# Optimization experiments

Measured on AMD Instinct MI355X. Metric: run time of the kernel, lower is better.

The kernel has to match this reference:

```python
import jax, jax.numpy as jnp
import numpy as np

GRID_SIZE = 5
ORDER = 3  # spline_order
H_STEP = 2.0 / GRID_SIZE  # grid_range = [-1, 1]
GRID = jnp.arange(-ORDER, GRID_SIZE + ORDER + 1, dtype=jnp.float32) * H_STEP - 1.0  # (12,)


def b_splines(x):
    # x: (N, F) -> bases: (N, F, GRID_SIZE + ORDER) via Cox-de Boor recursion
    g = GRID
    xx = x[..., None]
    bases = ((xx >= g[:-1]) & (xx < g[1:])).astype(x.dtype)
    for k in range(1, ORDER + 1):
        left = (xx - g[:-(k + 1)]) / (g[k:-1] - g[:-(k + 1)]) * bases[..., :-1]
        right = (g[k + 1:] - xx) / (g[k + 1:] - g[1:-k]) * bases[..., 1:]
        bases = left + right
    return bases


def kan_linear(x, bw, sw, sc):
    # x: (N, F); bw: (O, F); sw: (O, F, C); sc: (O, F)
    base = jax.nn.silu(x) @ bw.T
    spline = jnp.einsum('nfc,ofc->no', b_splines(x), sw * sc[..., None])
    return base + spline


def kan_conv(x, bw, sw, sc):
    # x: (B, C, H, W); 3x3 patches, padding 1, stride 1 -> KANLinear over C*9 features
    B, C, H, W = x.shape
    patches = jax.lax.conv_general_dilated_patches(x, (3, 3), (1, 1), ((1, 1), (1, 1)))  # (B, C*9, H, W)
    p = patches.transpose(0, 2, 3, 1).reshape(B * H * W, C * 9)
    o = kan_linear(p, bw, sw, sc)  # (B*H*W, Cout)
    return o.reshape(B, H, W, -1).transpose(0, 3, 1, 2)


def maxpool2(x):
    B, C, H, W = x.shape
    return x.reshape(B, C, H // 2, 2, W // 2, 2).max(axis=(3, 5))


def setup_inputs() -> dict:
    key = jax.random.key(0)
    ks = jax.random.split(key, 32)
    d = {}
    d['x'] = jax.random.normal(ks[0], (128, 3, 32, 32), dtype=jnp.float32)
    conv_specs = [(3, 4), (4, 8), (8, 16), (16, 32)]
    i = 1
    for li, (cin, cout) in enumerate(conv_specs, 1):
        fin = cin * 9
        d[f'bw{li}'] = jax.random.normal(ks[i], (cout, fin), dtype=jnp.float32) * (1.0 / np.sqrt(fin)); i += 1
        d[f'sw{li}'] = jax.random.normal(ks[i], (cout, fin, GRID_SIZE + ORDER), dtype=jnp.float32) * 0.1; i += 1
        d[f'sc{li}'] = jax.random.normal(ks[i], (cout, fin), dtype=jnp.float32) * (1.0 / np.sqrt(fin)); i += 1
    lin_specs = [(2048, 2048), (1024, 2048), (10, 1024)]
    for li, (o, inn) in enumerate(lin_specs, 1):
        d[f'w{li}'] = jax.random.normal(ks[i], (o, inn), dtype=jnp.float32) * (1.0 / np.sqrt(inn)); i += 1
        d[f'b{li}'] = jnp.zeros((o,), dtype=jnp.float32); i += 1
    return d


def reference(x, bw1, sw1, sc1, bw2, sw2, sc2, bw3, sw3, sc3, bw4, sw4, sc4, w1, b1, w2, b2, w3, b3):
    x = kan_conv(x, bw1, sw1, sc1)
    x = kan_conv(x, bw2, sw2, sc2)
    x = maxpool2(x)
    x = kan_conv(x, bw3, sw3, sc3)
    x = kan_conv(x, bw4, sw4, sc4)
    x = maxpool2(x)
    x = x.reshape(x.shape[0], -1)  # (B, 32*8*8)
    x = jax.nn.relu(x @ w1.T + b1)
    x = jax.nn.relu(x @ w2.T + b2)
    return x @ w3.T + b3
```

## Files before the change

kernel.cpp:

```cpp
#include <hip/hip_runtime.h>

#define BATCH 128
#define AST 88

typedef __attribute__((ext_vector_type(8))) short bf16x8;
typedef __attribute__((ext_vector_type(16))) float f32x16;

__device__ __forceinline__ void spline_acts(float xv, float act[9]) {
    act[0] = xv * (1.0f / (1.0f + __expf(-xv)));
    float g[12];
#pragma unroll
    for (int i = 0; i < 12; ++i) g[i] = (float)(i - 3) * 0.4f - 1.0f;
    float bb[11];
#pragma unroll
    for (int c = 0; c < 11; ++c) bb[c] = (xv >= g[c] && xv < g[c + 1]) ? 1.0f : 0.0f;
#pragma unroll
    for (int k = 1; k <= 3; ++k) {
#pragma unroll
        for (int c = 0; c + k < 11; ++c) {
            float left  = (xv - g[c]) * (1.0f / (g[c + k] - g[c])) * bb[c];
            float right = (g[c + k + 1] - xv) * (1.0f / (g[c + k + 1] - g[c + 1])) * bb[c + 1];
            bb[c] = left + right;
        }
    }
#pragma unroll
    for (int c = 0; c < 8; ++c) act[c + 1] = bb[c];
}

__device__ __constant__ float ZPAD[9] = {0.0f, 0.0f, 0.0f, 0.02083333333f,
                                         0.47916666667f, 0.47916666667f,
                                         0.02083333333f, 0.0f, 0.0f};

__device__ __forceinline__ void bf16split(float x, ushort& h, ushort& l) {
    union { float f; unsigned u; } a; a.f = x;
    unsigned r = a.u + 0x7FFF + ((a.u >> 16) & 1);
    h = (ushort)(r >> 16);
    union { unsigned u; float f; } hf; hf.u = (unsigned)h << 16;
    union { float f; unsigned u; } bres; bres.f = x - hf.f;
    unsigned r2 = bres.u + 0x7FFF + ((bres.u >> 16) & 1);
    l = (ushort)(r2 >> 16);
}

__device__ __forceinline__ float wval(const float* bw, const float* sw, const float* sc,
                                      int F, int f, int j, int o) {
    if (j == 0) return bw[o * F + f];
    return sw[(o * F + f) * 8 + (j - 1)] * sc[o * F + f];
}

__global__ void pack_frags(
    const float* __restrict__ bw1, const float* __restrict__ sw1, const float* __restrict__ sc1,
    const float* __restrict__ bw2, const float* __restrict__ sw2, const float* __restrict__ sc2,
    const float* __restrict__ bw3, const float* __restrict__ sw3, const float* __restrict__ sc3,
    const float* __restrict__ bw4, const float* __restrict__ sw4, const float* __restrict__ sc4,
    ushort* __restrict__ k1h, ushort* __restrict__ k1l,
    ushort* __restrict__ k2h, ushort* __restrict__ k2l,
    ushort* __restrict__ k3h, ushort* __restrict__ k3l,
    ushort* __restrict__ k4h, ushort* __restrict__ k4l,
    ushort* __restrict__ zph, ushort* __restrict__ zpl) {
    int i = blockIdx.x * 256 + threadIdx.x;
    if (i < 1152) {
        int l = i & 63, s = (i >> 6) & 1, t = i / 128;
#pragma unroll
        for (int e = 0; e < 8; ++e) {
            int k = s * 16 + ((l >> 5) * 8) + e, o = l & 31;
            float w = 0.f;
            if (k < 27 && o < 4) w = wval(bw1, sw1, sc1, 27, (k / 9) * 9 + t, k % 9, o);
            ushort h, lo; bf16split(w, h, lo);
            k1h[i * 8 + e] = h; k1l[i * 8 + e] = lo;
        }
    } else if (i < 2880) {
        int q = i - 1152;
        int l = q & 63, s = (q >> 6) % 3, t = q / 192;
#pragma unroll
        for (int e = 0; e < 8; ++e) {
            int k = s * 16 + ((l >> 5) * 8) + e, o = l & 31;
            float w = 0.f;
            if (k < 36 && o < 8) w = wval(bw2, sw2, sc2, 36, (k / 9) * 9 + t, k % 9, o);
            ushort h, lo; bf16split(w, h, lo);
            k2h[q * 8 + e] = h; k2l[q * 8 + e] = lo;
        }
    } else if (i < 5760) {
        int q = i - 2880;
        int l = q & 63, s = (q >> 6) % 5, t = q / 320;
#pragma unroll
        for (int e = 0; e < 8; ++e) {
            int k = s * 16 + ((l >> 5) * 8) + e, o = l & 31;
            float w = 0.f;
            if (k < 72 && o < 16) w = wval(bw3, sw3, sc3, 72, (k / 9) * 9 + t, k % 9, o);
            ushort h, lo; bf16split(w, h, lo);
            k3h[q * 8 + e] = h; k3l[q * 8 + e] = lo;
        }
    } else if (i < 11520) {
        int q = i - 5760;
        int l = q & 63, s = (q >> 6) % 5, t = (q / 320) % 9, p = q / 2880;
#pragma unroll
        for (int e = 0; e < 8; ++e) {
            int k = s * 16 + ((l >> 5) * 8) + e, o = l & 31;
            float w = 0.f;
            if (k < 72) w = wval(bw4, sw4, sc4, 144, (p * 8 + k / 9) * 9 + t, k % 9, o);
            ushort h, lo; bf16split(w, h, lo);
            k4h[q * 8 + e] = h; k4l[q * 8 + e] = lo;
        }
    } else if (i < 11600) {
        int c = i - 11520;
        ushort h, lo; bf16split(ZPAD[c % 9], h, lo);
        zph[c] = h; zpl[c] = lo;
    }
}

__global__ __launch_bounds__(256) void spline_x(const float* __restrict__ x,
                                                ushort* __restrict__ A1h,
                                                ushort* __restrict__ A1l) {
    __shared__ unsigned SB[7168];
    int i = blockIdx.x * 256 + threadIdx.x;
    int px = i & 1023, b = i >> 10;
    const float* xb = x + (size_t)b * 3072 + px;
    unsigned rh[14] = {}, rl[14] = {};
#pragma unroll
    for (int cin = 0; cin < 3; ++cin) {
        float a9[9];
        spline_acts(xb[cin * 1024], a9);
#pragma unroll
        for (int j = 0; j < 9; ++j) {
            ushort h, l2; bf16split(a9[j], h, l2);
            int c = cin * 9 + j;
            if (c & 1) { rh[c >> 1] |= (unsigned)h << 16; rl[c >> 1] |= (unsigned)l2 << 16; }
            else       { rh[c >> 1] |= h;                  rl[c >> 1] |= l2; }
        }
    }
    int wb = threadIdx.x * 14;
#pragma unroll
    for (int w = 0; w < 14; ++w) { SB[wb + w] = rh[w]; SB[3584 + wb + w] = rl[w]; }
    __syncthreads();
    const ushort* sb = (const ushort*)SB;
    size_t base = (size_t)blockIdx.x * 7168;
#pragma unroll
    for (int e = 0; e < 4; ++e) {
        int q = e * 256 + threadIdx.x;
        if (q < 896) {
            *(uint4*)(A1h + base + q * 8) = *(const uint4*)(sb + q * 8);
            *(uint4*)(A1l + base + q * 8) = *(const uint4*)(sb + 7168 + q * 8);
        }
    }
}

template <int KG, int CHG, int CHL, int ASTR, int KSTEPS, int NCO, int EPI>
__global__ __launch_bounds__(256) void conv_strip(
    const ushort* __restrict__ Agh, const ushort* __restrict__ Agl,
    const ushort* __restrict__ Bgh, const ushort* __restrict__ Bgl,
    const ushort* __restrict__ zph, const ushort* __restrict__ zpl,
    ushort* __restrict__ Oh, ushort* __restrict__ Ol) {
    __shared__ ushort AH[340 * ASTR];
    __shared__ ushort AL[340 * ASTR];
    const int tid = threadIdx.x;
    const int b = blockIdx.x >> 2, strip = blockIdx.x & 3;
    const int r0 = strip * 8;
    const int lane = tid & 63, wv = tid >> 6;

    {
        const ushort* ash = Agh + (size_t)b * 1024 * KG;
        const ushort* asl = Agl + (size_t)b * 1024 * KG;
        for (int idx = tid; idx < 320 * CHL; idx += 256) {
            int pxl = idx / CHL, ch = idx - pxl * CHL;
            int lr = pxl >> 5, c = pxl & 31;
            int grow = r0 - 1 + lr;
            uint2 vh, vl;
            if (ch >= CHG) { vh = make_uint2(0u, 0u); vl = make_uint2(0u, 0u); }
            else if ((unsigned)grow < 32u) {
                vh = *(const uint2*)(ash + (size_t)(grow * 32 + c) * KG + ch * 4);
                vl = *(const uint2*)(asl + (size_t)(grow * 32 + c) * KG + ch * 4);
            } else {
                vh = *(const uint2*)(zph + ch * 4);
                vl = *(const uint2*)(zpl + ch * 4);
            }
            int spx = lr * 34 + c + 1;
            *(uint2*)(&AH[spx * ASTR + ch * 4]) = vh;
            *(uint2*)(&AL[spx * ASTR + ch * 4]) = vl;
        }
        for (int idx = tid; idx < 20 * CHL; idx += 256) {
            int sel = idx / CHL, ch = idx - sel * CHL;
            int lr = sel >> 1, c = (sel & 1) ? 33 : 0;
            int spx = lr * 34 + c;
            uint2 vh, vl;
            if (ch >= CHG) { vh = make_uint2(0u, 0u); vl = make_uint2(0u, 0u); }
            else { vh = *(const uint2*)(zph + ch * 4); vl = *(const uint2*)(zpl + ch * 4); }
            *(uint2*)(&AH[spx * ASTR + ch * 4]) = vh;
            *(uint2*)(&AL[spx * ASTR + ch * 4]) = vl;
        }
    }
    __syncthreads();

    f32x16 acc0, acc1;
#pragma unroll
    for (int i = 0; i < 16; ++i) { acc0[i] = 0.f; acc1[i] = 0.f; }

    const int p0 = wv * 64 + (lane & 31);
    const int sp0 = ((p0 >> 5) + 1) * 34 + (p0 & 31) + 1;
    const int sp1 = sp0 + 34;
    const int koff = (lane >> 5) * 8;

#pragma unroll 1
    for (int t = 0; t < 9; ++t) {
        const int dA = ((t / 3) - 1) * 34 + (t % 3) - 1;
#pragma unroll
        for (int s = 0; s < KSTEPS; ++s) {
            bf16x8 a0h = *(const bf16x8*)(&AH[(sp0 + dA) * ASTR + s * 16 + koff]);
            bf16x8 a0l = *(const bf16x8*)(&AL[(sp0 + dA) * ASTR + s * 16 + koff]);
            bf16x8 a1h = *(const bf16x8*)(&AH[(sp1 + dA) * ASTR + s * 16 + koff]);
            bf16x8 a1l = *(const bf16x8*)(&AL[(sp1 + dA) * ASTR + s * 16 + koff]);
            bf16x8 bh = *(const bf16x8*)(Bgh + (size_t)((t * KSTEPS + s) * 64 + lane) * 8);
            bf16x8 bl = *(const bf16x8*)(Bgl + (size_t)((t * KSTEPS + s) * 64 + lane) * 8);
            acc0 = __builtin_amdgcn_mfma_f32_32x32x16_bf16(a0h, bh, acc0, 0, 0, 0);
            acc1 = __builtin_amdgcn_mfma_f32_32x32x16_bf16(a1h, bh, acc1, 0, 0, 0);
            acc0 = __builtin_amdgcn_mfma_f32_32x32x16_bf16(a0h, bl, acc0, 0, 0, 0);
            acc1 = __builtin_amdgcn_mfma_f32_32x32x16_bf16(a1h, bl, acc1, 0, 0, 0);
            acc0 = __builtin_amdgcn_mfma_f32_32x32x16_bf16(a0l, bh, acc0, 0, 0, 0);
            acc1 = __builtin_amdgcn_mfma_f32_32x32x16_bf16(a1l, bh, acc1, 0, 0, 0);
        }
    }
    __syncthreads();

    float* fl = (float*)AH;
    {
        int ccol = lane & 31;
        if (ccol < NCO) {
#pragma unroll
            for (int r = 0; r < 16; ++r) {
                int row = (r & 3) + 8 * (r >> 2) + 4 * (lane >> 5);
                fl[ccol * 257 + wv * 64 + row] = acc0[r];
                fl[ccol * 257 + wv * 64 + 32 + row] = acc1[r];
            }
        }
    }
    __syncthreads();

    if (EPI == 0) {
        unsigned* ubh = (unsigned*)AL;
        unsigned* ubl = (unsigned*)AH + 1032;
        unsigned rwh[18], rwl[18];
#pragma unroll
        for (int w = 0; w < 18; ++w) { rwh[w] = 0u; rwl[w] = 0u; }
#pragma unroll
        for (int co = 0; co < 4; ++co) {
            float a9[9];
            spline_acts(fl[co * 257 + tid], a9);
#pragma unroll
            for (int j = 0; j < 9; ++j) {
                ushort h, l2; bf16split(a9[j], h, l2);
                int c = co * 9 + j;
                if (c & 1) { rwh[c >> 1] |= (unsigned)h << 16; rwl[c >> 1] |= (unsigned)l2 << 16; }
                else       { rwh[c >> 1] |= h;                  rwl[c >> 1] |= l2; }
            }
        }
#pragma unroll
        for (int w = 0; w < 18; ++w) { ubh[tid * 18 + w] = rwh[w]; ubl[tid * 18 + w] = rwl[w]; }
        __syncthreads();
        size_t basew = ((size_t)b * 1024 + strip * 256) * 18;
        unsigned* goh = (unsigned*)Oh + basew;
        unsigned* gol = (unsigned*)Ol + basew;
#pragma unroll
        for (int e = 0; e < 18; ++e) {
            int q = e * 256 + tid;
            goh[q] = ubh[q];
            gol[q] = ubl[q];
        }
    } else {
        int cg = tid >> 6, pl = tid & 63;
        int phl = pl >> 4, pw = pl & 15;
        int base_m = (2 * phl) * 32 + 2 * pw;
        unsigned rwh[9], rwl[9];
#pragma unroll
        for (int w = 0; w < 9; ++w) { rwh[w] = 0u; rwl[w] = 0u; }
#pragma unroll
        for (int e = 0; e < 2; ++e) {
            int co = cg * 2 + e;
            const float* fb = fl + co * 257 + base_m;
            float m = fmaxf(fmaxf(fb[0], fb[1]), fmaxf(fb[32], fb[33]));
            float a9[9];
            spline_acts(m, a9);
#pragma unroll
            for (int j = 0; j < 9; ++j) {
                ushort h, l2; bf16split(a9[j], h, l2);
                int c = e * 9 + j;
                if (c & 1) { rwh[c >> 1] |= (unsigned)h << 16; rwl[c >> 1] |= (unsigned)l2 << 16; }
                else       { rwh[c >> 1] |= h;                  rwl[c >> 1] |= l2; }
            }
        }
        unsigned* ubh = (unsigned*)AL;
        unsigned* ubl = (unsigned*)AL + 2560;
#pragma unroll
        for (int w = 0; w < 9; ++w) {
            ubh[pl * 40 + cg * 9 + w] = rwh[w];
            ubl[pl * 40 + cg * 9 + w] = rwl[w];
        }
        if (cg == 3) {
#pragma unroll
            for (int w = 0; w < 4; ++w) { ubh[pl * 40 + 36 + w] = 0u; ubl[pl * 40 + 36 + w] = 0u; }
        }
        __syncthreads();
        size_t base = ((size_t)b * 256 + strip * 64) * 80;
        const ushort* sbh = (const ushort*)ubh;
        const ushort* sbl = (const ushort*)ubl;
#pragma unroll
        for (int e = 0; e < 3; ++e) {
            int q = e * 256 + tid;
            if (q < 640) {
                *(uint4*)(Oh + base + q * 8) = *(const uint4*)(sbh + q * 8);
                *(uint4*)(Ol + base + q * 8) = *(const uint4*)(sbl + q * 8);
            }
        }
    }
}

template <int NPH, int NCO>
__global__ __launch_bounds__(256) void conv34_part(
    const ushort* __restrict__ Agh, const ushort* __restrict__ Agl,
    const ushort* __restrict__ Bgh, const ushort* __restrict__ Bgl,
    const ushort* __restrict__ zph, const ushort* __restrict__ zpl,
    float* __restrict__ P) {
    __shared__ ushort AH[144 * AST];
    __shared__ ushort AL[144 * AST];
    const int tid = threadIdx.x;
    const int b = blockIdx.x, half = blockIdx.y, z = blockIdx.z;
    const int p = z / 3, g = z % 3;
    const int r0 = half * 8;
    const int lane = tid & 63, wv = tid >> 6;

    {
        const ushort* ash = Agh + ((size_t)b * NPH + p) * 256 * 80;
        const ushort* asl = Agl + ((size_t)b * NPH + p) * 256 * 80;
#pragma unroll
        for (int e = 0; e < 6; ++e) {
            int idx = e * 256 + tid;
            if (idx < 1440) {
                int px = idx / 10, ch = idx - px * 10;
                int pr = px / 18, pc = px - pr * 18;
                int r = r0 - 1 + g + pr, c = pc - 1;
                bool inb = ((unsigned)r < 16u) && ((unsigned)c < 16u);
                uint4 vh, vl;
                if (inb) {
                    vh = *(const uint4*)(ash + (size_t)(r * 16 + c) * 80 + ch * 8);
                    vl = *(const uint4*)(asl + (size_t)(r * 16 + c) * 80 + ch * 8);
                } else {
                    vh = *(const uint4*)(zph + ch * 8);
                    vl = *(const uint4*)(zpl + ch * 8);
                }
                *(uint4*)(&AH[px * AST + ch * 8]) = vh;
                *(uint4*)(&AL[px * AST + ch * 8]) = vl;
            }
        }
    }
    __syncthreads();

    f32x16 acc;
#pragma unroll
    for (int i = 0; i < 16; ++i) acc[i] = 0.f;

    const int m = wv * 32 + (lane & 31);
    const int sbase = (m >> 4) * 18 + (m & 15);
    const int koff = (lane >> 5) * 8;
    const ushort* bsh = Bgh + (size_t)p * 2880 * 8;
    const ushort* bsl = Bgl + (size_t)p * 2880 * 8;

#pragma unroll
    for (int dw = 0; dw < 3; ++dw) {
        const int t = g * 3 + dw;
#pragma unroll
        for (int s = 0; s < 5; ++s) {
            bf16x8 ah = *(const bf16x8*)(&AH[(sbase + dw) * AST + s * 16 + koff]);
            bf16x8 al = *(const bf16x8*)(&AL[(sbase + dw) * AST + s * 16 + koff]);
            bf16x8 bh = *(const bf16x8*)(bsh + (size_t)((t * 5 + s) * 64 + lane) * 8);
            bf16x8 bl = *(const bf16x8*)(bsl + (size_t)((t * 5 + s) * 64 + lane) * 8);
            acc = __builtin_amdgcn_mfma_f32_32x32x16_bf16(ah, bh, acc, 0, 0, 0);
            acc = __builtin_amdgcn_mfma_f32_32x32x16_bf16(ah, bl, acc, 0, 0, 0);
            acc = __builtin_amdgcn_mfma_f32_32x32x16_bf16(al, bh, acc, 0, 0, 0);
        }
    }

    int co = lane & 31;
    if (co < NCO) {
        float* pb = P + ((size_t)(z * 256 + b * 2 + half) * 128) * NCO;
#pragma unroll
        for (int r = 0; r < 16; ++r) {
            int px = wv * 32 + (r & 3) + 8 * (r >> 2) + 4 * (lane >> 5);
            pb[px * NCO + co] = acc[r];
        }
    }
}

__global__ __launch_bounds__(256) void conv3_reduce(const float* __restrict__ P3,
                                                    ushort* __restrict__ A4h,
                                                    ushort* __restrict__ A4l) {
    __shared__ ushort SBH[20480], SBL[20480];
    int b = blockIdx.x, p2 = blockIdx.y;
    int t = threadIdx.x;
    int co8 = t & 7, pxg = t >> 3;
    int co = p2 * 8 + co8;

#pragma unroll
    for (int q = 0; q < 8; ++q) {
        int px = pxg * 8 + q;
        int bh = b * 2 + (px >> 7), lpx = px & 127;
        float s = 0.f;
#pragma unroll
        for (int zz = 0; zz < 3; ++zz)
            s += P3[((size_t)(zz * 256 + bh) * 128 + lpx) * 16 + co];
        float a9[9];
        spline_acts(s, a9);
#pragma unroll
        for (int j = 0; j < 9; ++j) {
            ushort h, l2; bf16split(a9[j], h, l2);
            SBH[px * 80 + co8 * 9 + j] = h;
            SBL[px * 80 + co8 * 9 + j] = l2;
        }
        if (co8 == 7) {
#pragma unroll
            for (int w = 0; w < 8; ++w) { SBH[px * 80 + 72 + w] = 0; SBL[px * 80 + 72 + w] = 0; }
        }
    }
    __syncthreads();
    size_t base = ((size_t)(b * 2 + p2) * 256) * 80;
#pragma unroll
    for (int e = 0; e < 10; ++e) {
        int q = e * 256 + t;
        *(uint4*)(A4h + base + q * 8) = *(const uint4*)(SBH + q * 8);
        *(uint4*)(A4l + base + q * 8) = *(const uint4*)(SBL + q * 8);
    }
}

__global__ __launch_bounds__(256) void conv4_reduce_pool(const float* __restrict__ P4,
                                                         float* __restrict__ pooled) {
    __shared__ float SM[32 * 65];
    int b = blockIdx.x;
    int t = threadIdx.x;
    int co = t & 31, pg = t >> 5;
#pragma unroll
    for (int q = 0; q < 8; ++q) {
        int pp = pg * 8 + q;
        int pr = pp >> 3, pc = pp & 7;
        int half = pr >> 2, lr = pr & 3;
        int bh = b * 2 + half;
        int px00 = (2 * lr) * 16 + 2 * pc;
        float s00 = 0.f, s01 = 0.f, s10 = 0.f, s11 = 0.f;
#pragma unroll
        for (int zz = 0; zz < 6; ++zz) {
            const float* pb = P4 + ((size_t)(zz * 256 + bh) * 128) * 32 + co;
            s00 += pb[(size_t)px00 * 32];
            s01 += pb[(size_t)(px00 + 1) * 32];
            s10 += pb[(size_t)(px00 + 16) * 32];
            s11 += pb[(size_t)(px00 + 17) * 32];
        }
        SM[co * 65 + pp] = fmaxf(fmaxf(s00, s01), fmaxf(s10, s11));
    }
    __syncthreads();
#pragma unroll
    for (int e = 0; e < 8; ++e) {
        int idx = e * 256 + t;
        pooled[(size_t)b * 2048 + idx] = SM[(idx >> 6) * 65 + (idx & 63)];
    }
}

template <int SPLIT>
__global__ __launch_bounds__(256) void fc_big(const float* __restrict__ A,
                                              const float* __restrict__ Wt,
                                              float* __restrict__ part,
                                              int M, int N, int K) {
    __shared__ float As[32][68];
    __shared__ float Ws[32][68];
    const int tid = threadIdx.x;
    const int tx = tid & 15, ty = tid >> 4;
    const int bm = blockIdx.y * 64, bn = blockIdx.x * 64;
    const int kc = K / SPLIT;
    const int kbeg = blockIdx.z * kc;
    float acc[4][4] = {};
    for (int k0 = kbeg; k0 < kbeg + kc; k0 += 32) {
#pragma unroll
        for (int e = 0; e < 8; ++e) {
            int g = e * 256 + tid;
            int k = g & 31, r = g >> 5;
            As[k][r] = A[(size_t)(bm + r) * K + k0 + k];
            Ws[k][r] = Wt[(size_t)(bn + r) * K + k0 + k];
        }
        __syncthreads();
#pragma unroll
        for (int kk = 0; kk < 32; ++kk) {
            float4 av = *(const float4*)(&As[kk][ty * 4]);
            float4 wv = *(const float4*)(&Ws[kk][tx * 4]);
            acc[0][0] = fmaf(av.x, wv.x, acc[0][0]);
            acc[0][1] = fmaf(av.x, wv.y, acc[0][1]);
            acc[0][2] = fmaf(av.x, wv.z, acc[0][2]);
            acc[0][3] = fmaf(av.x, wv.w, acc[0][3]);
            acc[1][0] = fmaf(av.y, wv.x, acc[1][0]);
            acc[1][1] = fmaf(av.y, wv.y, acc[1][1]);
            acc[1][2] = fmaf(av.y, wv.z, acc[1][2]);
            acc[1][3] = fmaf(av.y, wv.w, acc[1][3]);
            acc[2][0] = fmaf(av.z, wv.x, acc[2][0]);
            acc[2][1] = fmaf(av.z, wv.y, acc[2][1]);
            acc[2][2] = fmaf(av.z, wv.z, acc[2][2]);
            acc[2][3] = fmaf(av.z, wv.w, acc[2][3]);
            acc[3][0] = fmaf(av.w, wv.x, acc[3][0]);
            acc[3][1] = fmaf(av.w, wv.y, acc[3][1]);
            acc[3][2] = fmaf(av.w, wv.z, acc[3][2]);
            acc[3][3] = fmaf(av.w, wv.w, acc[3][3]);
        }
        __syncthreads();
    }
    float* p = part + (size_t)blockIdx.z * M * N;
#pragma unroll
    for (int i = 0; i < 4; ++i) {
        float4 v = make_float4(acc[i][0], acc[i][1], acc[i][2], acc[i][3]);
        *(float4*)&p[(size_t)(bm + ty * 4 + i) * N + (bn + tx * 4)] = v;
    }
}

template <int SPLIT>
__global__ void fc_reduce(const float* __restrict__ part, const float* __restrict__ bias,
                          float* __restrict__ C, int MN, int N, int relu) {
    int i = blockIdx.x * 256 + threadIdx.x;
    if (i >= MN) return;
    float s = bias[i % N];
#pragma unroll
    for (int z = 0; z < SPLIT; ++z) s += part[(size_t)z * MN + i];
    C[i] = relu ? fmaxf(s, 0.f) : s;
}

__global__ __launch_bounds__(256) void fc3_kernel(const float* __restrict__ A,
                                                  const float* __restrict__ Wt,
                                                  const float* __restrict__ bias,
                                                  float* __restrict__ C) {
    int gid = blockIdx.x * 256 + threadIdx.x;
    int wid = gid >> 6;
    int lane = gid & 63;
    int m = wid / 10, n = wid - m * 10;
    const float4* a = (const float4*)(A + (size_t)m * 1024);
    const float4* w = (const float4*)(Wt + (size_t)n * 1024);
    float s = 0.f;
#pragma unroll
    for (int it = 0; it < 4; ++it) {
        float4 av = a[it * 64 + lane];
        float4 wv = w[it * 64 + lane];
        s += av.x * wv.x + av.y * wv.y + av.z * wv.z + av.w * wv.w;
    }
#pragma unroll
    for (int off = 32; off; off >>= 1) s += __shfl_xor(s, off);
    if (lane == 0) C[wid] = s + bias[n];
}

extern "C" void kernel_launch(void* const* d_in, const int* in_sizes, int n_in,
                              void* d_out, int out_size, void* d_ws, size_t ws_size,
                              hipStream_t stream) {
    const float* x   = (const float*)d_in[0];
    const float* bw1 = (const float*)d_in[1];
    const float* sw1 = (const float*)d_in[2];
    const float* sc1 = (const float*)d_in[3];
    const float* bw2 = (const float*)d_in[4];
    const float* sw2 = (const float*)d_in[5];
    const float* sc2 = (const float*)d_in[6];
    const float* bw3 = (const float*)d_in[7];
    const float* sw3 = (const float*)d_in[8];
    const float* sc3 = (const float*)d_in[9];
    const float* bw4 = (const float*)d_in[10];
    const float* sw4 = (const float*)d_in[11];
    const float* sc4 = (const float*)d_in[12];
    const float* w1  = (const float*)d_in[13];
    const float* b1  = (const float*)d_in[14];
    const float* w2  = (const float*)d_in[15];
    const float* b2  = (const float*)d_in[16];
    const float* w3  = (const float*)d_in[17];
    const float* b3  = (const float*)d_in[18];

    float*  wsf = (float*)d_ws;
    ushort* wsu = (ushort*)d_ws;
    ushort* k1h = wsu + 110848;
    ushort* k1l = wsu + 120064;
    ushort* k2h = wsu + 129280;
    ushort* k2l = wsu + 143104;
    ushort* k3h = wsu + 156928;
    ushort* k3l = wsu + 179968;
    ushort* k4h = wsu + 203008;
    ushort* k4l = wsu + 249088;
    ushort* zph = wsu + 295168;
    ushort* zpl = wsu + 295248;
    ushort* A1h = wsu + 524288;
    ushort* A1l = wsu + 4194304;
    ushort* A2h = wsu + 7864320;
    ushort* A2l = wsu + 12582912;
    ushort* A3h = wsu + 524288;
    ushort* A3l = wsu + 3145728;
    ushort* A4h = wsu + 5767168;
    ushort* A4l = wsu + 11010048;
    float* P3   = wsf + 9437184;
    float* P4   = wsf + 11534336;
    float* pooled = wsf + 262144;
    float* part1  = wsf + 524288;
    float* fc1o   = wsf + 2621440;
    float* part2  = wsf + 2883584;
    float* fc2o   = wsf + 3932160;

    pack_frags<<<46, 256, 0, stream>>>(bw1, sw1, sc1, bw2, sw2, sc2,
                                       bw3, sw3, sc3, bw4, sw4, sc4,
                                       k1h, k1l, k2h, k2l, k3h, k3l, k4h, k4l,
                                       zph, zpl);

    spline_x<<<512, 256, 0, stream>>>(x, A1h, A1l);
    conv_strip<28, 7, 8, 40, 2, 4, 0><<<512, 256, 0, stream>>>(A1h, A1l, k1h, k1l,
                                                               zph, zpl, A2h, A2l);
    conv_strip<36, 9, 12, 56, 3, 8, 1><<<512, 256, 0, stream>>>(A2h, A2l, k2h, k2l,
                                                                zph, zpl, A3h, A3l);
    conv34_part<1, 16><<<dim3(128, 2, 3), 256, 0, stream>>>(A3h, A3l, k3h, k3l,
                                                            zph, zpl, P3);
    conv3_reduce<<<dim3(128, 2), 256, 0, stream>>>(P3, A4h, A4l);
    conv34_part<2, 32><<<dim3(128, 2, 6), 256, 0, stream>>>(A4h, A4l, k4h, k4l,
                                                            zph, zpl, P4);
    conv4_reduce_pool<<<128, 256, 0, stream>>>(P4, pooled);

    fc_big<8><<<dim3(32, 2, 8), 256, 0, stream>>>(pooled, w1, part1, 128, 2048, 2048);
    fc_reduce<8><<<1024, 256, 0, stream>>>(part1, b1, fc1o, 262144, 2048, 1);
    fc_big<8><<<dim3(16, 2, 8), 256, 0, stream>>>(fc1o, w2, part2, 128, 1024, 2048);
    fc_reduce<8><<<512, 256, 0, stream>>>(part2, b2, fc2o, 131072, 1024, 1);
    fc3_kernel<<<320, 256, 0, stream>>>(fc2o, w3, b3, (float*)d_out);
}
```

Measured before the change: 152.4 us.

## Merge weight packing with spline prep, loop conv4 phases in-block, vectorize FC loads

Merges the weight-fragment packing kernel and the input spline kernel into one launch by giving extra blocks to the spline work, which removes a kernel launch. conv34_part now loops over the NPH channel phases inside each block and accumulates in registers. This halves the conv4 grid and the number of partial buffers the reduce kernel sums. The FC GEMM tile loader switches to float4 global loads with scattered shared-memory stores. Trade-offs: less parallelism in conv4, an extra barrier per phase, and possible LDS bank conflicts in the transposed stores.

```diff
diff --git a/kernel.cpp b/kernel.cpp
--- a/kernel.cpp
+++ b/kernel.cpp
@@ -47,7 +47,8 @@
     return sw[(o * F + f) * 8 + (j - 1)] * sc[o * F + f];
 }
 
-__global__ void pack_frags(
+__global__ __launch_bounds__(256) void prep_kernel(
+    const float* __restrict__ x,
     const float* __restrict__ bw1, const float* __restrict__ sw1, const float* __restrict__ sc1,
     const float* __restrict__ bw2, const float* __restrict__ sw2, const float* __restrict__ sc2,
     const float* __restrict__ bw3, const float* __restrict__ sw3, const float* __restrict__ sc3,
@@ -56,7 +57,43 @@
     ushort* __restrict__ k2h, ushort* __restrict__ k2l,
     ushort* __restrict__ k3h, ushort* __restrict__ k3l,
     ushort* __restrict__ k4h, ushort* __restrict__ k4l,
-    ushort* __restrict__ zph, ushort* __restrict__ zpl) {
+    ushort* __restrict__ zph, ushort* __restrict__ zpl,
+    ushort* __restrict__ A1h, ushort* __restrict__ A1l) {
+    __shared__ unsigned SB[7168];
+    if (blockIdx.x >= 46) {
+        int bid = blockIdx.x - 46;
+        int i = bid * 256 + threadIdx.x;
+        int px = i & 1023, b = i >> 10;
+        const float* xb = x + (size_t)b * 3072 + px;
+        unsigned rh[14] = {}, rl[14] = {};
+#pragma unroll
+        for (int cin = 0; cin < 3; ++cin) {
+            float a9[9];
+            spline_acts(xb[cin * 1024], a9);
+#pragma unroll
+            for (int j = 0; j < 9; ++j) {
+                ushort h, l2; bf16split(a9[j], h, l2);
+                int c = cin * 9 + j;
+                if (c & 1) { rh[c >> 1] |= (unsigned)h << 16; rl[c >> 1] |= (unsigned)l2 << 16; }
+                else       { rh[c >> 1] |= h;                  rl[c >> 1] |= l2; }
+            }
+        }
+        int wb = threadIdx.x * 14;
+#pragma unroll
+        for (int w = 0; w < 14; ++w) { SB[wb + w] = rh[w]; SB[3584 + wb + w] = rl[w]; }
+        __syncthreads();
+        const ushort* sb = (const ushort*)SB;
+        size_t base = (size_t)bid * 7168;
+#pragma unroll
+        for (int e = 0; e < 4; ++e) {
+            int q = e * 256 + threadIdx.x;
+            if (q < 896) {
+                *(uint4*)(A1h + base + q * 8) = *(const uint4*)(sb + q * 8);
+                *(uint4*)(A1l + base + q * 8) = *(const uint4*)(sb + 7168 + q * 8);
+            }
+        }
+        return;
+    }
     int i = blockIdx.x * 256 + threadIdx.x;
     if (i < 1152) {
         int l = i & 63, s = (i >> 6) & 1, t = i / 128;
@@ -105,42 +142,6 @@
         int c = i - 11520;
         ushort h, lo; bf16split(ZPAD[c % 9], h, lo);
         zph[c] = h; zpl[c] = lo;
-    }
-}
-
-__global__ __launch_bounds__(256) void spline_x(const float* __restrict__ x,
-                                                ushort* __restrict__ A1h,
-                                                ushort* __restrict__ A1l) {
-    __shared__ unsigned SB[7168];
-    int i = blockIdx.x * 256 + threadIdx.x;
-    int px = i & 1023, b = i >> 10;
-    const float* xb = x + (size_t)b * 3072 + px;
-    unsigned rh[14] = {}, rl[14] = {};
-#pragma unroll
-    for (int cin = 0; cin < 3; ++cin) {
-        float a9[9];
-        spline_acts(xb[cin * 1024], a9);
-#pragma unroll
-        for (int j = 0; j < 9; ++j) {
-            ushort h, l2; bf16split(a9[j], h, l2);
-            int c = cin * 9 + j;
-            if (c & 1) { rh[c >> 1] |= (unsigned)h << 16; rl[c >> 1] |= (unsigned)l2 << 16; }
-            else       { rh[c >> 1] |= h;                  rl[c >> 1] |= l2; }
-        }
-    }
-    int wb = threadIdx.x * 14;
-#pragma unroll
-    for (int w = 0; w < 14; ++w) { SB[wb + w] = rh[w]; SB[3584 + wb + w] = rl[w]; }
-    __syncthreads();
-    const ushort* sb = (const ushort*)SB;
-    size_t base = (size_t)blockIdx.x * 7168;
-#pragma unroll
-    for (int e = 0; e < 4; ++e) {
-        int q = e * 256 + threadIdx.x;
-        if (q < 896) {
-            *(uint4*)(A1h + base + q * 8) = *(const uint4*)(sb + q * 8);
-            *(uint4*)(A1l + base + q * 8) = *(const uint4*)(sb + 7168 + q * 8);
-        }
     }
 }
 
@@ -321,12 +322,21 @@
     __shared__ ushort AH[144 * AST];
     __shared__ ushort AL[144 * AST];
     const int tid = threadIdx.x;
-    const int b = blockIdx.x, half = blockIdx.y, z = blockIdx.z;
-    const int p = z / 3, g = z % 3;
+    const int b = blockIdx.x, half = blockIdx.y, g = blockIdx.z;
     const int r0 = half * 8;
     const int lane = tid & 63, wv = tid >> 6;
 
-    {
+    f32x16 acc;
+#pragma unroll
+    for (int i = 0; i < 16; ++i) acc[i] = 0.f;
+
+    const int m = wv * 32 + (lane & 31);
+    const int sbase = (m >> 4) * 18 + (m & 15);
+    const int koff = (lane >> 5) * 8;
+
+#pragma unroll 1
+    for (int p = 0; p < NPH; ++p) {
+        if (p) __syncthreads();
         const ushort* ash = Agh + ((size_t)b * NPH + p) * 256 * 80;
         const ushort* asl = Agl + ((size_t)b * NPH + p) * 256 * 80;
 #pragma unroll
@@ -349,37 +359,29 @@
                 *(uint4*)(&AL[px * AST + ch * 8]) = vl;
             }
         }
-    }
-    __syncthreads();
-
-    f32x16 acc;
-#pragma unroll
-    for (int i = 0; i < 16; ++i) acc[i] = 0.f;
-
-    const int m = wv * 32 + (lane & 31);
-    const int sbase = (m >> 4) * 18 + (m & 15);
-    const int koff = (lane >> 5) * 8;
-    const ushort* bsh = Bgh + (size_t)p * 2880 * 8;
-    const ushort* bsl = Bgl + (size_t)p * 2880 * 8;
-
-#pragma unroll
-    for (int dw = 0; dw < 3; ++dw) {
-        const int t = g * 3 + dw;
-#pragma unroll
-        for (int s = 0; s < 5; ++s) {
-            bf16x8 ah = *(const bf16x8*)(&AH[(sbase + dw) * AST + s * 16 + koff]);
-            bf16x8 al = *(const bf16x8*)(&AL[(sbase + dw) * AST + s * 16 + koff]);
-            bf16x8 bh = *(const bf16x8*)(bsh + (size_t)((t * 5 + s) * 64 + lane) * 8);
-            bf16x8 bl = *(const bf16x8*)(bsl + (size_t)((t * 5 + s) * 64 + lane) * 8);
-            acc = __builtin_amdgcn_mfma_f32_32x32x16_bf16(ah, bh, acc, 0, 0, 0);
-            acc = __builtin_amdgcn_mfma_f32_32x32x16_bf16(ah, bl, acc, 0, 0, 0);
-            acc = __builtin_amdgcn_mfma_f32_32x32x16_bf16(al, bh, acc, 0, 0, 0);
+        __syncthreads();
+
+        const ushort* bsh = Bgh + (size_t)p * 2880 * 8;
+        const ushort* bsl = Bgl + (size_t)p * 2880 * 8;
+#pragma unroll
+        for (int dw = 0; dw < 3; ++dw) {
+            const int t = g * 3 + dw;
+#pragma unroll
+            for (int s = 0; s < 5; ++s) {
+                bf16x8 ah = *(const bf16x8*)(&AH[(sbase + dw) * AST + s * 16 + koff]);
+                bf16x8 al = *(const bf16x8*)(&AL[(sbase + dw) * AST + s * 16 + koff]);
+                bf16x8 bh = *(const bf16x8*)(bsh + (size_t)((t * 5 + s) * 64 + lane) * 8);
+                bf16x8 bl = *(const bf16x8*)(bsl + (size_t)((t * 5 + s) * 64 + lane) * 8);
+                acc = __builtin_amdgcn_mfma_f32_32x32x16_bf16(ah, bh, acc, 0, 0, 0);
+                acc = __builtin_amdgcn_mfma_f32_32x32x16_bf16(ah, bl, acc, 0, 0, 0);
+                acc = __builtin_amdgcn_mfma_f32_32x32x16_bf16(al, bh, acc, 0, 0, 0);
+            }
         }
     }
 
     int co = lane & 31;
     if (co < NCO) {
-        float* pb = P + ((size_t)(z * 256 + b * 2 + half) * 128) * NCO;
+        float* pb = P + ((size_t)(g * 256 + b * 2 + half) * 128) * NCO;
 #pragma unroll
         for (int r = 0; r < 16; ++r) {
             int px = wv * 32 + (r & 3) + 8 * (r >> 2) + 4 * (lane >> 5);
@@ -443,7 +445,7 @@
         int px00 = (2 * lr) * 16 + 2 * pc;
         float s00 = 0.f, s01 = 0.f, s10 = 0.f, s11 = 0.f;
 #pragma unroll
-        for (int zz = 0; zz < 6; ++zz) {
+        for (int zz = 0; zz < 3; ++zz) {
             const float* pb = P4 + ((size_t)(zz * 256 + bh) * 128) * 32 + co;
             s00 += pb[(size_t)px00 * 32];
             s01 += pb[(size_t)(px00 + 1) * 32];
@@ -475,11 +477,15 @@
     float acc[4][4] = {};
     for (int k0 = kbeg; k0 < kbeg + kc; k0 += 32) {
 #pragma unroll
-        for (int e = 0; e < 8; ++e) {
-            int g = e * 256 + tid;
-            int k = g & 31, r = g >> 5;
-            As[k][r] = A[(size_t)(bm + r) * K + k0 + k];
-            Ws[k][r] = Wt[(size_t)(bn + r) * K + k0 + k];
+        for (int e = 0; e < 2; ++e) {
+            int q = e * 256 + tid;
+            int r = q >> 3, k4 = (q & 7) * 4;
+            float4 av = *(const float4*)&A[(size_t)(bm + r) * K + k0 + k4];
+            float4 wv = *(const float4*)&Wt[(size_t)(bn + r) * K + k0 + k4];
+            As[k4 + 0][r] = av.x; As[k4 + 1][r] = av.y;
+            As[k4 + 2][r] = av.z; As[k4 + 3][r] = av.w;
+            Ws[k4 + 0][r] = wv.x; Ws[k4 + 1][r] = wv.y;
+            Ws[k4 + 2][r] = wv.z; Ws[k4 + 3][r] = wv.w;
         }
         __syncthreads();
 #pragma unroll
@@ -597,12 +603,11 @@
     float* part2  = wsf + 2883584;
     float* fc2o   = wsf + 3932160;
 
-    pack_frags<<<46, 256, 0, stream>>>(bw1, sw1, sc1, bw2, sw2, sc2,
-                                       bw3, sw3, sc3, bw4, sw4, sc4,
-                                       k1h, k1l, k2h, k2l, k3h, k3l, k4h, k4l,
-                                       zph, zpl);
-
-    spline_x<<<512, 256, 0, stream>>>(x, A1h, A1l);
+    prep_kernel<<<558, 256, 0, stream>>>(x, bw1, sw1, sc1, bw2, sw2, sc2,
+                                         bw3, sw3, sc3, bw4, sw4, sc4,
+                                         k1h, k1l, k2h, k2l, k3h, k3l, k4h, k4l,
+                                         zph, zpl, A1h, A1l);
+
     conv_strip<28, 7, 8, 40, 2, 4, 0><<<512, 256, 0, stream>>>(A1h, A1l, k1h, k1l,
                                                                zph, zpl, A2h, A2l);
     conv_strip<36, 9, 12, 56, 3, 8, 1><<<512, 256, 0, stream>>>(A2h, A2l, k2h, k2l,
@@ -610,7 +615,7 @@
     conv34_part<1, 16><<<dim3(128, 2, 3), 256, 0, stream>>>(A3h, A3l, k3h, k3l,
                                                             zph, zpl, P3);
     conv3_reduce<<<dim3(128, 2), 256, 0, stream>>>(P3, A4h, A4l);
-    conv34_part<2, 32><<<dim3(128, 2, 6), 256, 0, stream>>>(A4h, A4l, k4h, k4l,
+    conv34_part<2, 32><<<dim3(128, 2, 3), 256, 0, stream>>>(A4h, A4l, k4h, k4l,
                                                             zph, zpl, P4);
     conv4_reduce_pool<<<128, 256, 0, stream>>>(P4, pooled);
 
```

Result: faster. 141.2 us (-7.4%).
